# Optimization experiments

Measured on AMD Instinct MI355X. Metric: run time of the kernel, lower is better.

## Reference

```python
import jax, jax.numpy as jnp
import numpy as np
import math

N_HEADS = 4
N_KV_GROUPS = 1
HEAD_DIM = 256
SLIDING_WINDOW = 512
ROPE_BASE = 1000000.0
EPS = 1e-6


def _rmsnorm(x, gamma):
    # normalize over last dim (head_dim), torch nn.RMSNorm semantics
    ms = jnp.mean(jnp.square(x), axis=-1, keepdims=True)
    return x * jax.lax.rsqrt(ms + EPS) * gamma


def _rope_tables(T, head_dim, dtype):
    inv_freq = 1.0 / (ROPE_BASE ** (jnp.arange(0, head_dim, 2, dtype=jnp.float32) / head_dim))
    t = jnp.arange(T, dtype=jnp.float32)
    freqs = jnp.outer(t, inv_freq)          # [T, head_dim/2]
    return jnp.cos(freqs).astype(dtype), jnp.sin(freqs).astype(dtype)


def _apply_rope(x, cos, sin):
    # x: [B, T, H, hd]; cos/sin: [T, hd/2] broadcast as [1, T, 1, hd/2]
    x0 = x[..., 0::2]
    x1 = x[..., 1::2]
    c = cos[None, :, None, :]
    s = sin[None, :, None, :]
    even = x0 * c - x1 * s
    odd = x0 * s + x1 * c
    return jnp.stack((even, odd), axis=-1).reshape(x.shape)


def setup_inputs() -> dict:
    key = jax.random.key(0)
    ks = jax.random.split(key, 5)
    B, T, C = 2, 4096, 1024
    scale = 0.02
    return {
        "x": jax.random.normal(ks[0], (B, T, C), dtype=jnp.float32),
        "Wq": jax.random.normal(ks[1], (C, C), dtype=jnp.float32) * scale,
        "Wk": jax.random.normal(ks[2], (N_KV_GROUPS * HEAD_DIM, C), dtype=jnp.float32) * scale,
        "Wv": jax.random.normal(ks[3], (N_KV_GROUPS * HEAD_DIM, C), dtype=jnp.float32) * scale,
        "Wo": jax.random.normal(ks[4], (C, C), dtype=jnp.float32) * scale,
        "q_gamma": jnp.ones((HEAD_DIM,), dtype=jnp.float32),
        "k_gamma": jnp.ones((HEAD_DIM,), dtype=jnp.float32),
    }


def reference(x, Wq, Wk, Wv, Wo, q_gamma, k_gamma):
    B, T, C = x.shape
    H, G, hd = N_HEADS, N_KV_GROUPS, HEAD_DIM
    rep = H // G

    q = (x @ Wq.T).reshape(B, T, H, hd)
    k = (x @ Wk.T).reshape(B, T, G, hd)
    v = (x @ Wv.T).reshape(B, T, G, hd)

    q = _rmsnorm(q, q_gamma)
    k = _rmsnorm(k, k_gamma)

    cos, sin = _rope_tables(T, hd, q.dtype)
    q = _apply_rope(q, cos, sin)
    k = _apply_rope(k, cos, sin)

    q = q.transpose(0, 2, 1, 3)                 # [B, H, T, hd]
    k = k.transpose(0, 2, 1, 3)                 # [B, G, T, hd]
    v = v.transpose(0, 2, 1, 3)
    k = jnp.repeat(k, rep, axis=1)              # [B, H, T, hd]
    v = jnp.repeat(v, rep, axis=1)

    scores = jnp.einsum("bhqd,bhkd->bhqk", q, k) / math.sqrt(hd)
    i = jnp.arange(T)[:, None]
    j = jnp.arange(T)[None, :]
    allowed = (j <= i) & (j >= i - SLIDING_WINDOW)   # causal sliding window
    scores = jnp.where(allowed, scores, -jnp.inf)
    attn = jax.nn.softmax(scores, axis=-1)
    out = jnp.einsum("bhqk,bhkd->bhqd", attn, v)     # [B, H, T, hd]
    out = out.transpose(0, 2, 1, 3).reshape(B, T, C)
    return out @ Wo.T
```

## Files before the change

kernel.cpp:

```cpp
#include <hip/hip_runtime.h>
#include <cstdint>
#include <cstddef>

#define T_SEQ 4096
#define NB    2
#define CDIM  1024
#define HD    256
#define NH    4

typedef __attribute__((ext_vector_type(8))) __bf16 bf16x8;
typedef __attribute__((ext_vector_type(4))) __bf16 bf16x4;
typedef __attribute__((ext_vector_type(4))) float  floatx4;

__device__ __forceinline__ floatx4 mfma16(bf16x8 a, bf16x8 b, floatx4 c) {
  return __builtin_amdgcn_mfma_f32_16x16x32_bf16(a, b, c, 0, 0, 0);
}

__device__ __forceinline__ void gl2lds16(const void* g, void* l) {
  __builtin_amdgcn_global_load_lds(
      (__attribute__((address_space(1))) void*)g,
      (__attribute__((address_space(3))) void*)l, 16, 0, 0);
}

__global__ __launch_bounds__(256) void cvt_all(const float* __restrict__ x,
                                               const float* __restrict__ wq,
                                               const float* __restrict__ wk,
                                               const float* __restrict__ wv,
                                               const float* __restrict__ wo,
                                               __bf16* __restrict__ xb,
                                               __bf16* __restrict__ wb,
                                               __bf16* __restrict__ wob) {
  int i = blockIdx.x * 256 + threadIdx.x;
  const float* src;
  __bf16* dst;
  int off;
  if (i < 2097152)      { src = x;  dst = xb;            off = i; }
  else if (i < 2359296) { src = wq; dst = wb;            off = i - 2097152; }
  else if (i < 2424832) { src = wk; dst = wb + 1048576;  off = i - 2359296; }
  else if (i < 2490368) { src = wv; dst = wb + 1310720;  off = i - 2424832; }
  else                  { src = wo; dst = wob;           off = i - 2490368; }
  float4 v = ((const float4*)src)[off];
  bf16x4 o;
  o[0] = (__bf16)v.x; o[1] = (__bf16)v.y; o[2] = (__bf16)v.z; o[3] = (__bf16)v.w;
  *(bf16x4*)&dst[(size_t)off * 4] = o;
}

template <typename OutT>
__global__ __launch_bounds__(256) void gemm_bt(const __bf16* __restrict__ A,
                                               const __bf16* __restrict__ B,
                                               OutT* __restrict__ C,
                                               int M, int N, int K) {
  __shared__ __bf16 As[128 * 64];
  __shared__ __bf16 Bs[128 * 64];
  const int tid  = threadIdx.x;
  const int lane = tid & 63;
  const int wave = tid >> 6;
  const int wm = wave >> 1, wn = wave & 1;
  const int lrow = lane & 15, quad = lane >> 4;
  const int bm = blockIdx.y, bn = blockIdx.x;

  const __bf16* gA = A + (size_t)(bm * 128) * K;
  const __bf16* gB = B + (size_t)(bn * 128) * K;
  const int arow = tid >> 3;
  const int acol = ((tid & 7) ^ ((tid >> 3) & 7)) * 8;
  const int l7 = lrow & 7;

  floatx4 acc[4][4] = {};

  for (int kt = 0; kt < K; kt += 64) {
#pragma unroll
    for (int i = 0; i < 4; ++i)
      gl2lds16(gA + (size_t)(i * 32 + arow) * K + kt + acol, &As[i * 2048 + tid * 8]);
#pragma unroll
    for (int i = 0; i < 4; ++i)
      gl2lds16(gB + (size_t)(i * 32 + arow) * K + kt + acol, &Bs[i * 2048 + tid * 8]);
    __syncthreads();
#pragma unroll
    for (int kk = 0; kk < 2; ++kk) {
      bf16x8 af[4], bfr[4];
#pragma unroll
      for (int mi = 0; mi < 4; ++mi)
        af[mi] = *(const bf16x8*)&As[(wm * 64 + mi * 16 + lrow) * 64 +
                                     ((kk * 4 + quad) ^ l7) * 8];
#pragma unroll
      for (int ni = 0; ni < 4; ++ni)
        bfr[ni] = *(const bf16x8*)&Bs[(wn * 64 + ni * 16 + lrow) * 64 +
                                      ((kk * 4 + quad) ^ l7) * 8];
#pragma unroll
      for (int mi = 0; mi < 4; ++mi)
#pragma unroll
        for (int ni = 0; ni < 4; ++ni)
          acc[mi][ni] = mfma16(af[mi], bfr[ni], acc[mi][ni]);
    }
    __syncthreads();
  }

  const int row0 = bm * 128 + wm * 64;
  const int col0 = bn * 128 + wn * 64;
#pragma unroll
  for (int mi = 0; mi < 4; ++mi)
#pragma unroll
    for (int ni = 0; ni < 4; ++ni)
#pragma unroll
      for (int r = 0; r < 4; ++r) {
        int row = row0 + mi * 16 + quad * 4 + r;
        int col = col0 + ni * 16 + lrow;
        C[(size_t)row * N + col] = (OutT)acc[mi][ni][r];
      }
}

__global__ __launch_bounds__(256) void rmsrope(const __bf16* __restrict__ qkv,
                                               const float* __restrict__ qg,
                                               const float* __restrict__ kg,
                                               __bf16* __restrict__ qr,
                                               __bf16* __restrict__ kr,
                                               __bf16* __restrict__ vt) {
  __shared__ __bf16 Ls[64 * 256];
  if (blockIdx.x >= 5120) {
    const int vb = blockIdx.x - 5120;
    const int b = vb >> 6, tt = vb & 63;
    const int tid = threadIdx.x;
    const __bf16* src = qkv + ((size_t)(b * 4096 + tt * 64)) * 1536 + 1280;
#pragma unroll
    for (int i = 0; i < 8; ++i)
      gl2lds16(src + (size_t)(i * 8 + (tid >> 5)) * 1536 + (tid & 31) * 8,
               &Ls[i * 2048 + tid * 8]);
    __syncthreads();
    __bf16 buf[64];
#pragma unroll
    for (int i = 0; i < 64; ++i) buf[i] = Ls[i * 256 + tid];
    __bf16* dst = vt + ((size_t)(b * 256 + tid)) * T_SEQ + tt * 64;
#pragma unroll
    for (int i = 0; i < 8; ++i)
      *(bf16x8*)&dst[i * 8] = *(const bf16x8*)&buf[i * 8];
    return;
  }

  const int inst = blockIdx.x * 4 + (threadIdx.x >> 6);
  const int lane = threadIdx.x & 63;
  const int rp = inst / 5, which = inst - rp * 5;
  const int row = rp * 2 + (lane >> 5);
  const int hl = lane & 31;
  const int b = row >> 12, t = row & 4095;

  const int srcoff = (which < 4) ? which * 256 : 1024;
  const __bf16* src = qkv + (size_t)row * 1536 + srcoff;
  bf16x8 xv = *(const bf16x8*)&src[hl * 8];

  float xf[8];
  float ss = 0.f;
#pragma unroll
  for (int j = 0; j < 8; ++j) { xf[j] = (float)xv[j]; ss += xf[j] * xf[j]; }
#pragma unroll
  for (int off = 16; off >= 1; off >>= 1) ss += __shfl_xor(ss, off);
  const float rms = rsqrtf(ss * (1.0f / 256.0f) + 1e-6f);

  const float* g = (which < 4) ? qg : kg;
  const float4 gv0 = *(const float4*)&g[hl * 8];
  const float4 gv1 = *(const float4*)&g[hl * 8 + 4];
  float y[8];
  y[0] = xf[0] * rms * gv0.x; y[1] = xf[1] * rms * gv0.y;
  y[2] = xf[2] * rms * gv0.z; y[3] = xf[3] * rms * gv0.w;
  y[4] = xf[4] * rms * gv1.x; y[5] = xf[5] * rms * gv1.y;
  y[6] = xf[6] * rms * gv1.z; y[7] = xf[7] * rms * gv1.w;

  const float c_log2 = -19.931568569324174f / 128.0f;
  bf16x8 ov;
#pragma unroll
  for (int j = 0; j < 4; ++j) {
    const int p = hl * 4 + j;
    const float a = (float)t * exp2f((float)p * c_log2);
    const float sn = __sinf(a), cs = __cosf(a);
    ov[2 * j]     = (__bf16)(y[2 * j] * cs - y[2 * j + 1] * sn);
    ov[2 * j + 1] = (__bf16)(y[2 * j] * sn + y[2 * j + 1] * cs);
  }

  __bf16* dst = (which < 4)
      ? qr + ((size_t)((b * NH + which) * T_SEQ) + t) * 256
      : kr + ((size_t)(b * T_SEQ) + t) * 256;
  *(bf16x8*)&dst[hl * 8] = ov;
}

__global__ __launch_bounds__(256, 2) void attn(const __bf16* __restrict__ qr,
                                               const __bf16* __restrict__ kr,
                                               const __bf16* __restrict__ vt,
                                               __bf16* __restrict__ ao) {
  __shared__ __bf16 Ks[2][64 * 256];
  __shared__ __bf16 Ps[2][64 * 64];

  const int bid = blockIdx.x;
  const int qi = bid & 63, h = (bid >> 6) & 3, b = bid >> 8;
  const int tid = threadIdx.x, wave = tid >> 6, lane = tid & 63;
  const int wq = wave & 1, wk = wave >> 1;
  const int lrow = lane & 15, quad = lane >> 4;
  const int l7 = lrow & 7;

  const __bf16* Q = qr + (size_t)((b * NH + h) * T_SEQ) * 256;
  const __bf16* K = kr + (size_t)(b * T_SEQ) * 256;
  const __bf16* V = vt + (size_t)(b * 256) * T_SEQ;

  const int qbase = qi * 64;

  bf16x8 qf[2][8];
#pragma unroll
  for (int qt = 0; qt < 2; ++qt)
#pragma unroll
    for (int c = 0; c < 8; ++c)
      qf[qt][c] = *(const bf16x8*)&Q[(size_t)(qbase + wq * 32 + qt * 16 + lrow) * 256 +
                                     c * 32 + quad * 8];

  bf16x8 onesv;
#pragma unroll
  for (int j = 0; j < 8; ++j) onesv[j] = (__bf16)1.0f;

  floatx4 o[2][8] = {};
  floatx4 lm[2] = {};

  const int jt0 = (qi >= 8) ? qi - 8 : 0;
  const int jt1 = qi;

  {
    const __bf16* Kt = K + (size_t)(jt0 * 64) * 256;
#pragma unroll
    for (int i = 0; i < 8; ++i)
      gl2lds16(Kt + (size_t)(i * 8 + (tid >> 5)) * 256 +
                   ((tid & 31) ^ ((tid >> 5) & 7)) * 8,
               &Ks[jt0 & 1][i * 2048 + tid * 8]);
  }
  if (jt1 > jt0) {
    const __bf16* Kt = K + (size_t)((jt0 + 1) * 64) * 256;
#pragma unroll
    for (int i = 0; i < 8; ++i)
      gl2lds16(Kt + (size_t)(i * 8 + (tid >> 5)) * 256 +
                   ((tid & 31) ^ ((tid >> 5) & 7)) * 8,
               &Ks[(jt0 + 1) & 1][i * 2048 + tid * 8]);
  }
  __syncthreads();

  for (int jt = jt0; jt <= jt1; ++jt) {
    const __bf16* Kb = Ks[jt & 1];
    __bf16* Pb = Ps[jt & 1];

    floatx4 s[2][2] = {};
#pragma unroll
    for (int c = 0; c < 8; ++c)
#pragma unroll
      for (int k16 = 0; k16 < 2; ++k16) {
        bf16x8 kf = *(const bf16x8*)&Kb[(wk * 32 + k16 * 16 + lrow) * 256 +
                                        ((c * 4 + quad) ^ l7) * 8];
#pragma unroll
        for (int qt = 0; qt < 2; ++qt)
          s[k16][qt] = mfma16(kf, qf[qt][c], s[k16][qt]);
      }

    const bool full = (jt < qi) && (jt >= qi - 7);

    const float C1 = 0.09016844005556021f;
    const float C2 = 23.083120654223415f;
#pragma unroll
    for (int k16 = 0; k16 < 2; ++k16)
#pragma unroll
      for (int qt = 0; qt < 2; ++qt) {
        bf16x4 pk;
#pragma unroll
        for (int r = 0; r < 4; ++r) {
          float v = s[k16][qt][r];
          if (!full) {
            const int jk = jt * 64 + wk * 32 + k16 * 16 + quad * 4 + r;
            const int iq = qbase + wq * 32 + qt * 16 + lrow;
            v = ((jk <= iq) && (jk + 512 >= iq)) ? v : -1e30f;
          }
          pk[r] = (__bf16)exp2f(v * C1 - C2);
        }
        const int q = wq * 32 + qt * 16 + lrow;
        const int chunk = (wk * 4 + k16 * 2 + (quad >> 1)) ^ l7;
        *(bf16x4*)((char*)Pb + q * 128 + chunk * 16 + (quad & 1) * 8) = pk;
      }
    __syncthreads();

    if (jt + 2 <= jt1) {
      const __bf16* Kt = K + (size_t)((jt + 2) * 64) * 256;
#pragma unroll
      for (int i = 0; i < 8; ++i)
        gl2lds16(Kt + (size_t)(i * 8 + (tid >> 5)) * 256 +
                     ((tid & 31) ^ ((tid >> 5) & 7)) * 8,
                 &Ks[jt & 1][i * 2048 + tid * 8]);
    }

    bf16x8 pf[2][2];
#pragma unroll
    for (int qt = 0; qt < 2; ++qt)
#pragma unroll
      for (int kc = 0; kc < 2; ++kc) {
        const int q = wq * 32 + qt * 16 + lrow;
        pf[qt][kc] = *(const bf16x8*)((char*)Pb + q * 128 +
                                      ((kc * 4 + quad) ^ l7) * 16);
      }

#pragma unroll
    for (int qt = 0; qt < 2; ++qt) {
      lm[qt] = mfma16(pf[qt][0], onesv, lm[qt]);
      lm[qt] = mfma16(pf[qt][1], onesv, lm[qt]);
    }

#pragma unroll
    for (int n = 0; n < 8; ++n)
#pragma unroll
      for (int kc = 0; kc < 2; ++kc) {
        bf16x8 vf = *(const bf16x8*)&V[(size_t)(wk * 128 + n * 16 + lrow) * T_SEQ +
                                       jt * 64 + kc * 32 + quad * 8];
        o[0][n] = mfma16(pf[0][kc], vf, o[0][n]);
        o[1][n] = mfma16(pf[1][kc], vf, o[1][n]);
      }
  }

#pragma unroll
  for (int qt = 0; qt < 2; ++qt)
#pragma unroll
    for (int r = 0; r < 4; ++r) {
      const float rl = 1.0f / lm[qt][r];
      const int tg = qbase + wq * 32 + qt * 16 + quad * 4 + r;
#pragma unroll
      for (int n = 0; n < 8; ++n)
        ao[((size_t)(b * T_SEQ + tg)) * CDIM + h * 256 + wk * 128 + n * 16 + lrow] =
            (__bf16)(o[qt][n][r] * rl);
    }
}

extern "C" void kernel_launch(void* const* d_in, const int* in_sizes, int n_in,
                              void* d_out, int out_size, void* d_ws, size_t ws_size,
                              hipStream_t stream) {
  const float* x  = (const float*)d_in[0];
  const float* Wq = (const float*)d_in[1];
  const float* Wk = (const float*)d_in[2];
  const float* Wv = (const float*)d_in[3];
  const float* Wo = (const float*)d_in[4];
  const float* qg = (const float*)d_in[5];
  const float* kg = (const float*)d_in[6];
  float* out = (float*)d_out;

  const size_t M = (size_t)NB * T_SEQ;
  char* ws = (char*)d_ws;
  __bf16* xb  = (__bf16*)ws; ws += M * CDIM * 2;
  __bf16* wb  = (__bf16*)ws; ws += (size_t)1536 * CDIM * 2;
  __bf16* wob = (__bf16*)ws; ws += (size_t)CDIM * CDIM * 2;
  __bf16* qkv = (__bf16*)ws; ws += M * 1536 * 2;
  __bf16* qr  = (__bf16*)ws; ws += M * CDIM * 2;
  __bf16* kr  = (__bf16*)ws; ws += M * HD * 2;
  __bf16* vt  = (__bf16*)ws; ws += M * HD * 2;
  __bf16* ao  = (__bf16*)ws;

  cvt_all<<<10752, 256, 0, stream>>>(x, Wq, Wk, Wv, Wo, xb, wb, wob);

  gemm_bt<__bf16><<<dim3(12, 64), 256, 0, stream>>>(xb, wb, qkv, 8192, 1536, 1024);

  rmsrope<<<5248, 256, 0, stream>>>(qkv, qg, kg, qr, kr, vt);

  attn<<<NB * NH * (T_SEQ / 64), 256, 0, stream>>>(qr, kr, vt, ao);

  gemm_bt<float><<<dim3(8, 64), 256, 0, stream>>>(ao, wob, out, 8192, 1024, 1024);
}
```

Before: 223.1 us.

## Stage V through LDS with smaller key tiles; direct-load A in GEMM

The attention kernel now uses 32-key tiles and double-buffers V tiles through LDS with a swizzled layout and async global-to-LDS loads, instead of reading V straight from global memory inside the PV loop. The GEMM drops the LDS staging of A, loading A fragments directly from global memory into registers, and double-buffers B in LDS so there is one barrier per k-step. It also raises the occupancy hint to 3 blocks. The aim is to cut global-load latency on the V path and shrink LDS use and barriers in the GEMM. The trade-offs are twice as many attention iterations and barriers, and A reads in the GEMM that are not staged or coalesced through LDS.

```diff
diff --git a/kernel.cpp b/kernel.cpp
--- a/kernel.cpp
+++ b/kernel.cpp
@@ -46,53 +46,65 @@
 }
 
 template <typename OutT>
-__global__ __launch_bounds__(256) void gemm_bt(const __bf16* __restrict__ A,
-                                               const __bf16* __restrict__ B,
-                                               OutT* __restrict__ C,
-                                               int M, int N, int K) {
-  __shared__ __bf16 As[128 * 64];
-  __shared__ __bf16 Bs[128 * 64];
+__global__ __launch_bounds__(256, 3) void gemm_bt(const __bf16* __restrict__ A,
+                                                  const __bf16* __restrict__ B,
+                                                  OutT* __restrict__ C,
+                                                  int M, int N, int K) {
+  __shared__ __bf16 Bs[2][128 * 64];
   const int tid  = threadIdx.x;
   const int lane = tid & 63;
   const int wave = tid >> 6;
   const int wm = wave >> 1, wn = wave & 1;
   const int lrow = lane & 15, quad = lane >> 4;
+  const int l7 = lrow & 7;
   const int bm = blockIdx.y, bn = blockIdx.x;
 
   const __bf16* gA = A + (size_t)(bm * 128) * K;
   const __bf16* gB = B + (size_t)(bn * 128) * K;
   const int arow = tid >> 3;
   const int acol = ((tid & 7) ^ ((tid >> 3) & 7)) * 8;
-  const int l7 = lrow & 7;
 
   floatx4 acc[4][4] = {};
-
-  for (int kt = 0; kt < K; kt += 64) {
-#pragma unroll
-    for (int i = 0; i < 4; ++i)
-      gl2lds16(gA + (size_t)(i * 32 + arow) * K + kt + acol, &As[i * 2048 + tid * 8]);
-#pragma unroll
-    for (int i = 0; i < 4; ++i)
-      gl2lds16(gB + (size_t)(i * 32 + arow) * K + kt + acol, &Bs[i * 2048 + tid * 8]);
+  const int nkt = K >> 6;
+
+#pragma unroll
+  for (int i = 0; i < 4; ++i)
+    gl2lds16(gB + (size_t)(i * 32 + arow) * K + acol, &Bs[0][i * 2048 + tid * 8]);
+
+  for (int kt = 0; kt < nkt; ++kt) {
     __syncthreads();
+
+    if (kt + 1 < nkt) {
+      const __bf16* src = gB + (kt + 1) * 64;
+#pragma unroll
+      for (int i = 0; i < 4; ++i)
+        gl2lds16(src + (size_t)(i * 32 + arow) * K + acol,
+                 &Bs[(kt + 1) & 1][i * 2048 + tid * 8]);
+    }
+
+    const __bf16* Ab = gA + kt * 64;
+    bf16x8 af[2][4];
+#pragma unroll
+    for (int kk = 0; kk < 2; ++kk)
+#pragma unroll
+      for (int mi = 0; mi < 4; ++mi)
+        af[kk][mi] = *(const bf16x8*)&Ab[(size_t)(wm * 64 + mi * 16 + lrow) * K +
+                                         kk * 32 + quad * 8];
+
+    const __bf16* Bb = Bs[kt & 1];
 #pragma unroll
     for (int kk = 0; kk < 2; ++kk) {
-      bf16x8 af[4], bfr[4];
+      bf16x8 bfr[4];
+#pragma unroll
+      for (int ni = 0; ni < 4; ++ni)
+        bfr[ni] = *(const bf16x8*)&Bb[(wn * 64 + ni * 16 + lrow) * 64 +
+                                      ((kk * 4 + quad) ^ l7) * 8];
 #pragma unroll
       for (int mi = 0; mi < 4; ++mi)
-        af[mi] = *(const bf16x8*)&As[(wm * 64 + mi * 16 + lrow) * 64 +
-                                     ((kk * 4 + quad) ^ l7) * 8];
-#pragma unroll
-      for (int ni = 0; ni < 4; ++ni)
-        bfr[ni] = *(const bf16x8*)&Bs[(wn * 64 + ni * 16 + lrow) * 64 +
-                                      ((kk * 4 + quad) ^ l7) * 8];
-#pragma unroll
-      for (int mi = 0; mi < 4; ++mi)
 #pragma unroll
         for (int ni = 0; ni < 4; ++ni)
-          acc[mi][ni] = mfma16(af[mi], bfr[ni], acc[mi][ni]);
-    }
-    __syncthreads();
+          acc[mi][ni] = mfma16(af[kk][mi], bfr[ni], acc[mi][ni]);
+    }
   }
 
   const int row0 = bm * 128 + wm * 64;
@@ -185,8 +197,9 @@
                                                const __bf16* __restrict__ kr,
                                                const __bf16* __restrict__ vt,
                                                __bf16* __restrict__ ao) {
-  __shared__ __bf16 Ks[2][64 * 256];
-  __shared__ __bf16 Ps[2][64 * 64];
+  __shared__ __bf16 Ks[2][32 * 256];
+  __shared__ __bf16 Vs[2][256 * 32];
+  __shared__ __bf16 Ps[2][64 * 32];
 
   const int bid = blockIdx.x;
   const int qi = bid & 63, h = (bid >> 6) & 3, b = bid >> 8;
@@ -216,102 +229,97 @@
   floatx4 o[2][8] = {};
   floatx4 lm[2] = {};
 
-  const int jt0 = (qi >= 8) ? qi - 8 : 0;
-  const int jt1 = qi;
-
-  {
-    const __bf16* Kt = K + (size_t)(jt0 * 64) * 256;
-#pragma unroll
-    for (int i = 0; i < 8; ++i)
-      gl2lds16(Kt + (size_t)(i * 8 + (tid >> 5)) * 256 +
-                   ((tid & 31) ^ ((tid >> 5) & 7)) * 8,
-               &Ks[jt0 & 1][i * 2048 + tid * 8]);
-  }
-  if (jt1 > jt0) {
-    const __bf16* Kt = K + (size_t)((jt0 + 1) * 64) * 256;
-#pragma unroll
-    for (int i = 0; i < 8; ++i)
-      gl2lds16(Kt + (size_t)(i * 8 + (tid >> 5)) * 256 +
-                   ((tid & 31) ^ ((tid >> 5) & 7)) * 8,
-               &Ks[(jt0 + 1) & 1][i * 2048 + tid * 8]);
-  }
+  const int jt0 = (qi >= 8) ? 2 * qi - 16 : 0;
+  const int jt1 = 2 * qi + 1;
+
+  const int krow = tid >> 5;
+  const int kcol = ((tid & 31) ^ (krow & 7)) * 8;
+  const int vrow = tid >> 2;
+  const int vcol = ((tid & 3) ^ ((vrow ^ (vrow >> 2)) & 3)) * 8;
+
+#pragma unroll
+  for (int i = 0; i < 4; ++i)
+    gl2lds16(K + (size_t)(jt0 * 32 + i * 8 + krow) * 256 + kcol,
+             &Ks[jt0 & 1][i * 2048 + tid * 8]);
+#pragma unroll
+  for (int i = 0; i < 4; ++i)
+    gl2lds16(K + (size_t)((jt0 + 1) * 32 + i * 8 + krow) * 256 + kcol,
+             &Ks[(jt0 + 1) & 1][i * 2048 + tid * 8]);
+#pragma unroll
+  for (int i = 0; i < 4; ++i)
+    gl2lds16(V + (size_t)(i * 64 + vrow) * T_SEQ + jt0 * 32 + vcol,
+             &Vs[jt0 & 1][i * 2048 + tid * 8]);
   __syncthreads();
 
   for (int jt = jt0; jt <= jt1; ++jt) {
     const __bf16* Kb = Ks[jt & 1];
-    __bf16* Pb = Ps[jt & 1];
-
-    floatx4 s[2][2] = {};
-#pragma unroll
-    for (int c = 0; c < 8; ++c)
-#pragma unroll
-      for (int k16 = 0; k16 < 2; ++k16) {
-        bf16x8 kf = *(const bf16x8*)&Kb[(wk * 32 + k16 * 16 + lrow) * 256 +
-                                        ((c * 4 + quad) ^ l7) * 8];
-#pragma unroll
-        for (int qt = 0; qt < 2; ++qt)
-          s[k16][qt] = mfma16(kf, qf[qt][c], s[k16][qt]);
-      }
-
-    const bool full = (jt < qi) && (jt >= qi - 7);
+
+    floatx4 s[2] = {};
+#pragma unroll
+    for (int c = 0; c < 8; ++c) {
+      bf16x8 kf = *(const bf16x8*)&Kb[(wk * 16 + lrow) * 256 +
+                                      ((c * 4 + quad) ^ l7) * 8];
+      s[0] = mfma16(kf, qf[0][c], s[0]);
+      s[1] = mfma16(kf, qf[1][c], s[1]);
+    }
+
+    const bool full = (jt <= 2 * qi - 1) && (jt >= 2 * qi - 14);
 
     const float C1 = 0.09016844005556021f;
     const float C2 = 23.083120654223415f;
-#pragma unroll
-    for (int k16 = 0; k16 < 2; ++k16)
-#pragma unroll
-      for (int qt = 0; qt < 2; ++qt) {
-        bf16x4 pk;
-#pragma unroll
-        for (int r = 0; r < 4; ++r) {
-          float v = s[k16][qt][r];
-          if (!full) {
-            const int jk = jt * 64 + wk * 32 + k16 * 16 + quad * 4 + r;
-            const int iq = qbase + wq * 32 + qt * 16 + lrow;
-            v = ((jk <= iq) && (jk + 512 >= iq)) ? v : -1e30f;
-          }
-          pk[r] = (__bf16)exp2f(v * C1 - C2);
+    __bf16* Pb = Ps[jt & 1];
+#pragma unroll
+    for (int qt = 0; qt < 2; ++qt) {
+      bf16x4 pk;
+#pragma unroll
+      for (int r = 0; r < 4; ++r) {
+        float v = s[qt][r];
+        if (!full) {
+          const int jk = jt * 32 + wk * 16 + quad * 4 + r;
+          const int iq = qbase + wq * 32 + qt * 16 + lrow;
+          v = ((jk <= iq) && (jk + 512 >= iq)) ? v : -1e30f;
         }
-        const int q = wq * 32 + qt * 16 + lrow;
-        const int chunk = (wk * 4 + k16 * 2 + (quad >> 1)) ^ l7;
-        *(bf16x4*)((char*)Pb + q * 128 + chunk * 16 + (quad & 1) * 8) = pk;
+        pk[r] = (__bf16)exp2f(v * C1 - C2);
       }
+      const int q = wq * 32 + qt * 16 + lrow;
+      const int chunk = (wk * 2 + (quad >> 1)) ^ ((q ^ (q >> 2)) & 3);
+      *(bf16x4*)((char*)Pb + q * 64 + chunk * 16 + (quad & 1) * 8) = pk;
+    }
     __syncthreads();
 
     if (jt + 2 <= jt1) {
-      const __bf16* Kt = K + (size_t)((jt + 2) * 64) * 256;
-#pragma unroll
-      for (int i = 0; i < 8; ++i)
-        gl2lds16(Kt + (size_t)(i * 8 + (tid >> 5)) * 256 +
-                     ((tid & 31) ^ ((tid >> 5) & 7)) * 8,
+#pragma unroll
+      for (int i = 0; i < 4; ++i)
+        gl2lds16(K + (size_t)((jt + 2) * 32 + i * 8 + krow) * 256 + kcol,
                  &Ks[jt & 1][i * 2048 + tid * 8]);
     }
-
-    bf16x8 pf[2][2];
-#pragma unroll
-    for (int qt = 0; qt < 2; ++qt)
-#pragma unroll
-      for (int kc = 0; kc < 2; ++kc) {
-        const int q = wq * 32 + qt * 16 + lrow;
-        pf[qt][kc] = *(const bf16x8*)((char*)Pb + q * 128 +
-                                      ((kc * 4 + quad) ^ l7) * 16);
-      }
-
+    if (jt + 1 <= jt1) {
+#pragma unroll
+      for (int i = 0; i < 4; ++i)
+        gl2lds16(V + (size_t)(i * 64 + vrow) * T_SEQ + (jt + 1) * 32 + vcol,
+                 &Vs[(jt + 1) & 1][i * 2048 + tid * 8]);
+    }
+
+    bf16x8 pf[2];
 #pragma unroll
     for (int qt = 0; qt < 2; ++qt) {
-      lm[qt] = mfma16(pf[qt][0], onesv, lm[qt]);
-      lm[qt] = mfma16(pf[qt][1], onesv, lm[qt]);
-    }
-
-#pragma unroll
-    for (int n = 0; n < 8; ++n)
-#pragma unroll
-      for (int kc = 0; kc < 2; ++kc) {
-        bf16x8 vf = *(const bf16x8*)&V[(size_t)(wk * 128 + n * 16 + lrow) * T_SEQ +
-                                       jt * 64 + kc * 32 + quad * 8];
-        o[0][n] = mfma16(pf[0][kc], vf, o[0][n]);
-        o[1][n] = mfma16(pf[1][kc], vf, o[1][n]);
-      }
+      const int q = wq * 32 + qt * 16 + lrow;
+      pf[qt] = *(const bf16x8*)((char*)Pb + q * 64 +
+                                (quad ^ ((q ^ (q >> 2)) & 3)) * 16);
+    }
+
+    lm[0] = mfma16(pf[0], onesv, lm[0]);
+    lm[1] = mfma16(pf[1], onesv, lm[1]);
+
+    const __bf16* Vb = Vs[jt & 1];
+#pragma unroll
+    for (int n = 0; n < 8; ++n) {
+      const int row = wk * 128 + n * 16 + lrow;
+      bf16x8 vf = *(const bf16x8*)&Vb[row * 32 +
+                                      ((quad ^ ((row ^ (row >> 2)) & 3)) * 8)];
+      o[0][n] = mfma16(pf[0], vf, o[0][n]);
+      o[1][n] = mfma16(pf[1], vf, o[1][n]);
+    }
   }
 
 #pragma unroll
```

After: 246.9 us. 10.7% more time.
